# Optimization experiments

Hardware: AMD Instinct MI355X
Metric: run time of the kernel (lower is better)

The kernel has to match this reference:

```python
import jax, jax.numpy as jnp
import numpy as np

B, S, L, C, H, W_IMG = 4, 2, 1024, 128, 256, 256
HEADS1, D1 = 4, C // 4          # layer 1: 4 heads x 32 dims, concat
HEADS2, D2 = 1, C               # layer 2: 1 head x 128 dims, mean
LN_EPS = 1e-5
NEG_SLOPE = 0.2


def _xavier(k, shape):
    limit = float(np.sqrt(6.0 / (shape[0] + shape[1])))
    return jax.random.uniform(k, shape, jnp.float32, -limit, limit)


def setup_inputs() -> dict:
    key = jax.random.key(0)
    ks = jax.random.split(key, 10)
    seg_feats = jax.random.normal(ks[0], (B, S, L, C), jnp.float32)
    # integer segment labels in 0..L (0 = background), stored per forward spec
    seg_images = jax.random.randint(ks[1], (B, S, H, W_IMG), 0, L + 1, jnp.int32)
    seg_nums = jnp.full((B, S), L, jnp.int32)
    return {
        "seg_feats": seg_feats,
        "seg_images": seg_images,
        "seg_nums": seg_nums,
        "W1": _xavier(ks[2], (HEADS1 * D1, C)),   # Linear weight (out, in)
        "a_src1": _xavier(ks[3], (HEADS1, D1)),
        "a_dst1": _xavier(ks[4], (HEADS1, D1)),
        "W2": _xavier(ks[5], (HEADS2 * D2, C)),
        "a_src2": _xavier(ks[6], (HEADS2, D2)),
        "a_dst2": _xavier(ks[7], (HEADS2, D2)),
        "ln_gamma": jnp.ones((C,), jnp.float32),
        "ln_beta": jnp.zeros((C,), jnp.float32),
    }


def build_adjacency(seg):
    """seg: (H, W) int labels in 1..L (0 = background) -> (L, L) float adj with self-loops."""
    adj = jnp.eye(L, dtype=jnp.float32)

    def add_edges(adj, a, b):
        valid = (a > 0) & (b > 0) & (a != b)
        ai = jnp.clip(a - 1, 0, L - 1)
        bi = jnp.clip(b - 1, 0, L - 1)
        v = valid.astype(jnp.float32)
        adj = adj.at[ai, bi].max(v)
        return adj.at[bi, ai].max(v)

    pairs = [
        (seg[:, :-1], seg[:, 1:]),       # horizontal
        (seg[:-1, :], seg[1:, :]),       # vertical
        (seg[:-1, :-1], seg[1:, 1:]),    # diagonal \
        (seg[:-1, 1:], seg[1:, :-1]),    # diagonal /
    ]
    for a, b in pairs:
        adj = add_edges(adj, a.reshape(-1), b.reshape(-1))
    return adj


def _leaky_relu(x):
    return jnp.where(x >= 0, x, NEG_SLOPE * x)


def gat_layer(x, adj, W, a_src, a_dst, heads, d, concat):
    N = x.shape[0]
    Wf = (x @ W.T).reshape(N, heads, d)                     # (N, h, d)
    e_src = jnp.einsum('nhd,hd->nh', Wf, a_src)             # (N, h)
    e_dst = jnp.einsum('nhd,hd->nh', Wf, a_dst)             # (N, h)
    e = _leaky_relu(e_src[:, None, :] + e_dst[None, :, :])  # (N, N, h)
    e = jnp.where((adj == 0)[:, :, None], -jnp.inf, e)
    alpha = jax.nn.softmax(e, axis=1)                       # softmax over neighbours j
    h = jnp.einsum('ijh,jhd->ihd', alpha, Wf)               # (N, h, d)
    if concat:
        return jax.nn.elu(h.reshape(N, heads * d))
    return h.mean(axis=1)


def reference(seg_feats, seg_images, seg_nums, W1, a_src1, a_dst1,
              W2, a_src2, a_dst2, ln_gamma, ln_beta):
    feats = seg_feats.reshape(B * S, L, C)
    adjs = jax.vmap(build_adjacency)(seg_images.reshape(B * S, H, W_IMG))

    def enrich(f, adj):
        h = gat_layer(f, adj, W1, a_src1, a_dst1, HEADS1, D1, True)
        h = gat_layer(h, adj, W2, a_src2, a_dst2, HEADS2, D2, False)
        y = f + h
        mu = jnp.mean(y, axis=-1, keepdims=True)
        var = jnp.var(y, axis=-1, keepdims=True)
        return (y - mu) * jax.lax.rsqrt(var + LN_EPS) * ln_gamma + ln_beta

    out = jax.vmap(enrich)(feats, adjs)
    return out.reshape(B, S, L, C)
```

## Files before the change

### kernel.cpp

```cpp
#include <hip/hip_runtime.h>
#include <hip/hip_bf16.h>
#include <stdint.h>

#define LL 1024
#define CC 128
#define NG 8
#define NN (NG*LL)
typedef __hip_bfloat16 bf16;
typedef __attribute__((ext_vector_type(8))) short short8;
typedef __attribute__((ext_vector_type(4))) short short4v;
typedef __attribute__((ext_vector_type(4))) float f32x4;

__device__ __forceinline__ bool is_bf16_wire(const void* gamma) {
  return *(const uint32_t*)gamma == 0x3F803F80u;
}
__device__ __forceinline__ float ldw(const void* p, size_t i, bool bf) {
  return bf ? __bfloat162float(((const bf16*)p)[i]) : ((const float*)p)[i];
}
__device__ __forceinline__ uint32_t encf(float f) {
  uint32_t b = __float_as_uint(f);
  return (b & 0x80000000u) ? ~b : (b | 0x80000000u);
}
__device__ __forceinline__ float decf(uint32_t u) {
  return (u & 0x80000000u) ? __uint_as_float(u & 0x7FFFFFFFu) : __uint_as_float(~u);
}
__device__ __forceinline__ short f2bs(float x) {
  uint32_t u = __float_as_uint(x);
  u += 0x7FFFu + ((u >> 16) & 1u);
  return (short)(u >> 16);
}
template <bool BFW>
__device__ __forceinline__ short8 ld8w(const void* p, size_t off) {
  if (BFW) {
    return *(const short8*)((const bf16*)p + off);
  } else {
    const float4* f = (const float4*)((const float*)p + off);
    float4 a = f[0], b = f[1];
    short8 r;
    r[0] = f2bs(a.x); r[1] = f2bs(a.y); r[2] = f2bs(a.z); r[3] = f2bs(a.w);
    r[4] = f2bs(b.x); r[5] = f2bs(b.y); r[6] = f2bs(b.z); r[7] = f2bs(b.w);
    return r;
  }
}


template <int NH, bool BFW>
__device__ __forceinline__ void gemm_split(const short8 af[4],
    const void* __restrict__ Wsrc, const void* __restrict__ as_,
    const void* __restrict__ ad_, bf16* __restrict__ WfT,
    float* __restrict__ es, float* __restrict__ ed,
    uint32_t* __restrict__ edmax, int n0, int lane, int w,
    float* __restrict__ lds_red) {
  int quad = lane >> 4, c = lane & 15;
  int g = n0 >> 10;
  int dt0 = w * 2;
  f32x4 acc[2];
  acc[0] = (f32x4){0.f, 0.f, 0.f, 0.f};
  acc[1] = (f32x4){0.f, 0.f, 0.f, 0.f};
#pragma unroll
  for (int ks = 0; ks < 4; ks++)
#pragma unroll
    for (int d2 = 0; d2 < 2; d2++) {
      short8 bfr = ld8w<BFW>(Wsrc, (size_t)((dt0 + d2) * 16 + c) * CC + ks * 32 + quad * 8);
      acc[d2] = __builtin_amdgcn_mfma_f32_16x16x32_bf16(af[ks], bfr, acc[d2], 0, 0, 0);
    }
  {
    int nw4 = ((n0 & 1023) >> 2) + quad;
    bf16* wdst = WfT + (size_t)g * 131072 + (size_t)nw4 * 512 + c * 4;
#pragma unroll
    for (int d2 = 0; d2 < 2; d2++) {
      short4v pk;
#pragma unroll
      for (int r = 0; r < 4; r++) pk[r] = f2bs(acc[d2][r]);
      *(short4v*)&wdst[(dt0 + d2) * 64] = pk;
    }
  }
  float sv[4] = {0.f, 0.f, 0.f, 0.f}, dv[4] = {0.f, 0.f, 0.f, 0.f};
#pragma unroll
  for (int d2 = 0; d2 < 2; d2++) {
    int o = (dt0 + d2) * 16 + c;
    float a_s = ldw(as_, o, BFW);
    float a_d = ldw(ad_, o, BFW);
#pragma unroll
    for (int r = 0; r < 4; r++) {
      sv[r] += acc[d2][r] * a_s;
      dv[r] += acc[d2][r] * a_d;
    }
  }
#pragma unroll
  for (int m = 1; m <= 8; m <<= 1)
#pragma unroll
    for (int r = 0; r < 4; r++) {
      sv[r] += __shfl_xor(sv[r], m);
      dv[r] += __shfl_xor(dv[r], m);
    }
  if (NH == 4) {
    if (c == 0)
#pragma unroll
      for (int r = 0; r < 4; r++) {
        int node = n0 + quad * 4 + r;
        es[node * 4 + w] = sv[r];
        ed[node * 4 + w] = dv[r];
      }
    float mq = fmaxf(fmaxf(dv[0], dv[1]), fmaxf(dv[2], dv[3]));
    mq = fmaxf(mq, __shfl_xor(mq, 16));
    mq = fmaxf(mq, __shfl_xor(mq, 32));
    if (lane == 0) atomicMax(&edmax[g * 4 + w], encf(mq));
  } else {
    if (c == 0)
#pragma unroll
      for (int r = 0; r < 4; r++) {
        int nl = quad * 4 + r;
        lds_red[(w * 16 + nl) * 2 + 0] = sv[r];
        lds_red[(w * 16 + nl) * 2 + 1] = dv[r];
      }
    __syncthreads();
    if (w == 0) {
      int nl = lane & 15;
      float se = 0.f, de = 0.f;
#pragma unroll
      for (int ww = 0; ww < 4; ww++) {
        se += lds_red[(ww * 16 + nl) * 2 + 0];
        de += lds_red[(ww * 16 + nl) * 2 + 1];
      }
      if (lane < 16) { es[n0 + nl] = se; ed[n0 + nl] = de; }
      float mq = de;
      mq = fmaxf(mq, __shfl_xor(mq, 1));
      mq = fmaxf(mq, __shfl_xor(mq, 2));
      mq = fmaxf(mq, __shfl_xor(mq, 4));
      mq = fmaxf(mq, __shfl_xor(mq, 8));
      if (lane == 0) atomicMax(&edmax[g], encf(mq));
    }
  }
}

template <bool BFW>
__device__ __forceinline__ void gemm1_body(const void* __restrict__ feats,
    const void* __restrict__ W1, const void* __restrict__ as1,
    const void* __restrict__ ad1, bf16* __restrict__ WfT,
    float* __restrict__ es, float* __restrict__ ed,
    uint32_t* __restrict__ edmax, int bb, int t) {
  int lane = t & 63, w = t >> 6;
  int quad = lane >> 4, c = lane & 15;
  int n0 = (bb & 7) * 1024 + (bb >> 3) * 16;
  short8 af[4];
#pragma unroll
  for (int ks = 0; ks < 4; ks++)
    af[ks] = ld8w<BFW>(feats, (size_t)(n0 + c) * CC + ks * 32 + quad * 8);
  gemm_split<4, BFW>(af, W1, as1, ad1, WfT, es, ed, edmax, n0, lane, w, nullptr);
}

__global__ __launch_bounds__(256) void k_front(
    const void* __restrict__ feats, const void* __restrict__ W1,
    const void* __restrict__ as1, const void* __restrict__ ad1,
    const void* __restrict__ gamma, const int* __restrict__ img,
    uint8_t* __restrict__ adj, bf16* __restrict__ WfT,
    float* __restrict__ es, float* __restrict__ ed,
    uint32_t* __restrict__ edmax) {
  int bid = blockIdx.x;
  if (bid < 512) {
    if (is_bf16_wire(gamma))
      gemm1_body<true>(feats, W1, as1, ad1, WfT, es, ed, edmax, bid, threadIdx.x);
    else
      gemm1_body<false>(feats, W1, as1, ad1, WfT, es, ed, edmax, bid, threadIdx.x);
    return;
  }
  int rel = bid - 512;
  int g = rel & 7;
  int y = rel >> 3;
  int x = threadIdx.x;
  int p = y * 256 + x;
  const int* im = img + g * 65536;
  uint8_t* A = adj + ((size_t)g << 20);
  int a = im[p];
  if (a > 0) {
    int nxs[4] = {x + 1, x, x + 1, x - 1};
    int nys[4] = {y, y + 1, y + 1, y + 1};
#pragma unroll
    for (int d = 0; d < 4; d++) {
      int nx = nxs[d], ny = nys[d];
      if (nx < 0 || nx > 255 || ny > 255) continue;
      int b = im[ny * 256 + nx];
      if (b > 0 && b != a) {
        A[(size_t)(a - 1) * LL + (b - 1)] = 1;
      }
    }
  }
}

template <int NH>
__global__ __launch_bounds__(256) void k_attn(
    const bf16* __restrict__ WfT, const float* __restrict__ esb,
    const float* __restrict__ edb, const uint8_t* __restrict__ adjb,
    const uint32_t* __restrict__ edmax, bf16* __restrict__ pacc,
    float* __restrict__ pml) {
  __shared__ __align__(16) float smem[8320];
  __shared__ float lred[4][16 * NH];
  uint8_t* scol = (uint8_t*)smem;
  float* eds = smem + 2560;
  float* red = smem;
  int t = threadIdx.x;
  int lane = t & 63, w = t >> 6;
  int quad = lane >> 4, c = lane & 15;
  int bid = blockIdx.x;
  int g = bid & 7, jp = (bid >> 3) & 1, rt = bid >> 4;
  int i0 = rt * 16;
  int node = g * LL + i0 + c;
  int J0 = jp * 512 + w * 128;
  for (int u = t; u < 512 * NH; u += 256) {
    int h = u >> 9, j = u & 511;
    eds[h * 520 + j] = edb[(size_t)(g * LL + jp * 512 + j) * NH + h];
  }
  for (int u = t; u < 512; u += 256) {
    const uint8_t* src = adjb + ((size_t)g << 20) + (size_t)(jp * 512 + u) * 1024 + i0;
    uint4 v = *(const uint4*)src;
    uint32_t* dst = (uint32_t*)&scol[u * 20];
    dst[0] = v.x; dst[1] = v.y; dst[2] = v.z; dst[3] = v.w;
  }
  const float LOG2E = 1.44269504f;
  float esv[NH], cmv[NH];
  if (NH == 4) {
    const float4 e4 = *(const float4*)&esb[(size_t)node * 4];
    esv[0] = e4.x; esv[1] = e4.y; esv[2] = e4.z; esv[3] = e4.w;
  } else {
    esv[0] = esb[node];
  }
#pragma unroll
  for (int h = 0; h < NH; h++) {
    float mx = decf(edmax[NH == 4 ? g * 4 + h : g]);
    float m = esv[h] + mx; m = fmaxf(m, 0.2f * m);
    cmv[h] = -m * LOG2E;
  }
  int rowg = i0 + c;
  const uint8_t* arow = adjb + ((size_t)g << 20) + (size_t)rowg * 1024 + jp * 512 + w * 128;
  uint2 mbj[4];
#pragma unroll
  for (int jb = 0; jb < 4; jb++)
    mbj[jb] = *(const uint2*)&arow[jb * 32 + quad * 8];
  f32x4 acc[8];
#pragma unroll
  for (int dt = 0; dt < 8; dt++) acc[dt] = (f32x4){0.f, 0.f, 0.f, 0.f};
  float lsum[NH];
#pragma unroll
  for (int h = 0; h < NH; h++) lsum[h] = 0.f;
  const bf16* wb = WfT + (size_t)g * 131072 + (size_t)J0 * 128 + quad * 1024 + c * 4;
  __syncthreads();

  union FB { uint2 u[2]; short8 s; };
#pragma unroll
  for (int jb = 0; jb < 4; jb++) {
    short8 frag[8];
#pragma unroll
    for (int dt = 0; dt < 8; dt++) {
      FB f;
      f.u[0] = *(const uint2*)&wb[jb * 4096 + dt * 64];
      f.u[1] = *(const uint2*)&wb[jb * 4096 + dt * 64 + 512];
      frag[dt] = f.s;
    }
    int base_wj = w * 128 + jb * 32 + quad * 8;
    int jg0 = jp * 512 + base_wj;
    uint32_t bx = mbj[jb].x, by = mbj[jb].y;
    float mf[8];
#pragma unroll
    for (int i = 0; i < 8; i++) {
      uint32_t bit = (i < 4) ? ((bx >> (8 * i)) & 1u) : ((by >> (8 * (i - 4))) & 1u);
      uint32_t cb = scol[(base_wj + i) * 20 + c];
      uint32_t mm = bit | cb | (uint32_t)(jg0 + i == rowg);
      mf[i] = (float)(mm != 0u);
    }
#pragma unroll
    for (int h = 0; h < NH; h++) {
      const float* ep = &eds[h * 520 + base_wj];
      float4 ea = *(const float4*)ep;
      float4 eb = *(const float4*)(ep + 4);
      float ev[8] = {ea.x, ea.y, ea.z, ea.w, eb.x, eb.y, eb.z, eb.w};
      float pr[8];
      float lac = 0.f;
#pragma unroll
      for (int i = 0; i < 8; i++) {
        float e = esv[h] + ev[i];
        e = fmaxf(e, 0.2f * e);
        float p = exp2f(fmaf(e, LOG2E, cmv[h]));
        p *= mf[i];
        lac += p;
        pr[i] = p;
      }
      lsum[h] += lac;
      union { short8 s; uint32_t u[4]; } A;
#pragma unroll
      for (int k = 0; k < 4; k++) {
        __hip_bfloat162 q = __float22bfloat162_rn(make_float2(pr[2*k], pr[2*k+1]));
        A.u[k] = *reinterpret_cast<uint32_t*>(&q);
      }
#pragma unroll
      for (int d2 = 0; d2 < 8 / NH; d2++) {
        int dt = h * (8 / NH) + d2;
        acc[dt] = __builtin_amdgcn_mfma_f32_16x16x32_bf16(A.s, frag[dt], acc[dt], 0, 0, 0);
      }
    }
  }
#pragma unroll
  for (int h = 0; h < NH; h++) {
    float v = lsum[h];
    v += __shfl_xor(v, 16);
    v += __shfl_xor(v, 32);
    lsum[h] = v;
  }
  if (quad == 0)
#pragma unroll
    for (int h = 0; h < NH; h++) lred[w][c * NH + h] = lsum[h];
  __syncthreads();
  if (w >= 1)
#pragma unroll
    for (int dt = 0; dt < 8; dt++)
      *(f32x4*)&red[(w - 1) * 2048 + dt * 256 + lane * 4] = acc[dt];
  __syncthreads();
  if (w == 0) {
#pragma unroll
    for (int dt = 0; dt < 8; dt++) {
      acc[dt] += *(const f32x4*)&red[dt * 256 + lane * 4];
      acc[dt] += *(const f32x4*)&red[2048 + dt * 256 + lane * 4];
      acc[dt] += *(const f32x4*)&red[4096 + dt * 256 + lane * 4];
    }
#pragma unroll
    for (int dt = 0; dt < 8; dt++)
#pragma unroll
      for (int r = 0; r < 4; r++)
        red[6144 + (quad * 4 + r) * 132 + dt * 16 + c] = acc[dt][r];
  }
  __syncthreads();
  {
    int row = t >> 4, d0 = (t & 15) * 8;
    const float* src = &red[6144 + row * 132 + d0];
    short8 pk;
#pragma unroll
    for (int k = 0; k < 8; k++) pk[k] = f2bs(src[k]);
    *(short8*)&pacc[((size_t)jp * NN + g * LL + i0 + row) * CC + d0] = pk;
  }
  if (t < 16 * NH) {
    float l = lred[0][t] + lred[1][t] + lred[2][t] + lred[3][t];
    int row = (NH == 4) ? (t >> 2) : t;
    int h = (NH == 4) ? (t & 3) : 0;
    if (NH == 4) pml[((size_t)jp * NN + g * LL + i0 + row) * 4 + h] = l;
    else         pml[(size_t)jp * NN + g * LL + i0 + row] = l;
  }
}

template <bool BFW>
__device__ __forceinline__ void gemm2_body(const bf16* __restrict__ pacc,
    const float* __restrict__ pml1, const void* __restrict__ W2,
    const void* __restrict__ as2, const void* __restrict__ ad2,
    bf16* __restrict__ WfT, float* __restrict__ es, float* __restrict__ ed,
    uint32_t* __restrict__ edmax, float* __restrict__ lds_red,
    int bid, int t) {
  int lane = t & 63, w = t >> 6;
  int quad = lane >> 4, c = lane & 15;
  int n0 = (bid & 7) * 1024 + (bid >> 3) * 16;
  int node = n0 + c;
  float4 l4 = make_float4(0.f, 0.f, 0.f, 0.f);
#pragma unroll
  for (int p = 0; p < 2; p++) {
    float4 v = *(const float4*)&pml1[((size_t)p * NN + node) * 4];
    l4.x += v.x; l4.y += v.y; l4.z += v.z; l4.w += v.w;
  }
  float linv[4] = {1.f / l4.x, 1.f / l4.y, 1.f / l4.z, 1.f / l4.w};
  short8 af[4];
#pragma unroll
  for (int ks = 0; ks < 4; ks++) {
    float a[8] = {0.f, 0.f, 0.f, 0.f, 0.f, 0.f, 0.f, 0.f};
#pragma unroll
    for (int p = 0; p < 2; p++) {
      short8 v = *(const short8*)&pacc[((size_t)p * NN + node) * CC + ks * 32 + quad * 8];
#pragma unroll
      for (int i = 0; i < 8; i++) {
        union { short s[2]; float f; } cv; cv.s[0] = 0; cv.s[1] = v[i];
        a[i] += cv.f;
      }
    }
#pragma unroll
    for (int i = 0; i < 8; i++) {
      float vv = a[i] * linv[ks];
      vv = (vv > 0.f) ? vv : (__expf(vv) - 1.f);
      af[ks][i] = f2bs(vv);
    }
  }
  gemm_split<1, BFW>(af, W2, as2, ad2, WfT, es, ed, edmax, n0, lane, w, lds_red);
}

__global__ __launch_bounds__(256) void k_gemm2c(
    const bf16* __restrict__ pacc, const float* __restrict__ pml1,
    const void* __restrict__ W2, const void* __restrict__ as2,
    const void* __restrict__ ad2, const void* __restrict__ gamma,
    bf16* __restrict__ WfT, float* __restrict__ es, float* __restrict__ ed,
    uint32_t* __restrict__ edmax) {
  __shared__ float lds_red[128];
  if (is_bf16_wire(gamma))
    gemm2_body<true>(pacc, pml1, W2, as2, ad2, WfT, es, ed, edmax, lds_red,
                     blockIdx.x, threadIdx.x);
  else
    gemm2_body<false>(pacc, pml1, W2, as2, ad2, WfT, es, ed, edmax, lds_red,
                      blockIdx.x, threadIdx.x);
}

__global__ __launch_bounds__(256) void k_combine2(const bf16* __restrict__ pacc,
    const float* __restrict__ pml2, const void* __restrict__ feats,
    const void* __restrict__ gamma, const void* __restrict__ beta,
    void* __restrict__ outp) {
  const bool bf = is_bf16_wire(gamma);
  int t = threadIdx.x;
  int node = (blockIdx.x & 7) * 1024 + (blockIdx.x >> 3) * 4 + (t >> 6);
  int lane = t & 63;
  float l = 0.f, a0 = 0.f, a1 = 0.f;
#pragma unroll
  for (int p = 0; p < 2; p++) {
    l  += pml2[(size_t)p * NN + node];
    a0 += __bfloat162float(pacc[((size_t)p * NN + node) * CC + lane]);
    a1 += __bfloat162float(pacc[((size_t)p * NN + node) * CC + 64 + lane]);
  }
  float y0 = ldw(feats, (size_t)node * CC + lane, bf) + a0 / l;
  float y1 = ldw(feats, (size_t)node * CC + 64 + lane, bf) + a1 / l;
  float s = y0 + y1, s2 = y0 * y0 + y1 * y1;
#pragma unroll
  for (int mm = 32; mm >= 1; mm >>= 1) { s += __shfl_xor(s, mm); s2 += __shfl_xor(s2, mm); }
  float mu = s * (1.f / 128.f);
  float var = fmaxf(s2 * (1.f / 128.f) - mu * mu, 0.f);
  float rs = rsqrtf(var + 1e-5f);
  float o0 = (y0 - mu) * rs * ldw(gamma, lane, bf) + ldw(beta, lane, bf);
  float o1 = (y1 - mu) * rs * ldw(gamma, 64 + lane, bf) + ldw(beta, 64 + lane, bf);
  if (bf) {
    ((bf16*)outp)[(size_t)node * CC + lane]      = __float2bfloat16(o0);
    ((bf16*)outp)[(size_t)node * CC + 64 + lane] = __float2bfloat16(o1);
  } else {
    ((float*)outp)[(size_t)node * CC + lane]      = o0;
    ((float*)outp)[(size_t)node * CC + 64 + lane] = o1;
  }
}

extern "C" void kernel_launch(void* const* d_in, const int* in_sizes, int n_in,
                              void* d_out, int out_size, void* d_ws, size_t ws_size,
                              hipStream_t stream) {
  const void* feats = d_in[0];
  const int*  imgs  = (const int*)d_in[1];
  const void* W1    = d_in[3];
  const void* as1   = d_in[4];
  const void* ad1   = d_in[5];
  const void* W2    = d_in[6];
  const void* as2   = d_in[7];
  const void* ad2   = d_in[8];
  const void* gamma = d_in[9];
  const void* beta  = d_in[10];

  char* ws = (char*)d_ws;
  uint8_t*  adj    = (uint8_t*)ws;
  uint32_t* edmax1 = (uint32_t*)(ws + 8388608);
  uint32_t* edmax2 = (uint32_t*)(ws + 8388736);
  bf16*     WfT    = (bf16*)(ws + 8519680);
  float*    es1    = (float*)(ws + 10616832);
  float*    ed1    = (float*)(ws + 10747904);
  float*    es2    = (float*)(ws + 10878976);
  float*    ed2    = (float*)(ws + 10911744);
  float*    pml    = (float*)(ws + 10944512);
  bf16*     pacc   = (bf16*)(ws + 11206656);

  hipMemsetAsync(ws, 0, 8389120, stream);
  hipLaunchKernelGGL(k_front, dim3(2560), dim3(256), 0, stream,
                     feats, W1, as1, ad1, gamma, imgs,
                     adj, WfT, es1, ed1, edmax1);
  hipLaunchKernelGGL((k_attn<4>), dim3(1024), dim3(256), 0, stream,
                     WfT, es1, ed1, adj, edmax1, pacc, pml);
  hipLaunchKernelGGL(k_gemm2c, dim3(512), dim3(256), 0, stream,
                     pacc, pml, W2, as2, ad2, gamma, WfT, es2, ed2, edmax2);
  hipLaunchKernelGGL((k_attn<1>), dim3(1024), dim3(256), 0, stream,
                     WfT, es2, ed2, adj, edmax2, pacc, pml);
  hipLaunchKernelGGL(k_combine2, dim3(2048), dim3(256), 0, stream,
                     pacc, pml, feats, gamma, beta, d_out);
}
```

Before: 168.1 us.

## Symmetrize adjacency at build time and process two row tiles per attention block

The adjacency builder now writes both (a,b) and (b,a) entries, so the attention kernel no longer stages a transposed column slice of the mask in shared memory and ORs it in. Each attention block now covers 32 query rows (two 16-row MFMA tiles) instead of 16. The WfT fragments and destination scores loaded per block are shared across both tiles, and the grid is halved. The trade-off is twice the scattered byte writes in the adjacency build and more accumulator registers per thread (two sets of 8 f32x4), which may reduce occupancy. The epilogue reduction now runs once per tile with extra barriers.

```diff
diff --git a/kernel.cpp b/kernel.cpp
--- a/kernel.cpp
+++ b/kernel.cpp
@@ -183,6 +183,7 @@
       int b = im[ny * 256 + nx];
       if (b > 0 && b != a) {
         A[(size_t)(a - 1) * LL + (b - 1)] = 1;
+        A[(size_t)(b - 1) * LL + (a - 1)] = 1;
       }
     }
   }
@@ -195,54 +196,54 @@
     const uint32_t* __restrict__ edmax, bf16* __restrict__ pacc,
     float* __restrict__ pml) {
   __shared__ __align__(16) float smem[8320];
-  __shared__ float lred[4][16 * NH];
-  uint8_t* scol = (uint8_t*)smem;
-  float* eds = smem + 2560;
+  __shared__ float lred[2][4][16 * NH];
+  float* eds = smem;
   float* red = smem;
   int t = threadIdx.x;
   int lane = t & 63, w = t >> 6;
   int quad = lane >> 4, c = lane & 15;
   int bid = blockIdx.x;
   int g = bid & 7, jp = (bid >> 3) & 1, rt = bid >> 4;
-  int i0 = rt * 16;
-  int node = g * LL + i0 + c;
+  int i0 = rt * 32;
   int J0 = jp * 512 + w * 128;
   for (int u = t; u < 512 * NH; u += 256) {
     int h = u >> 9, j = u & 511;
     eds[h * 520 + j] = edb[(size_t)(g * LL + jp * 512 + j) * NH + h];
   }
-  for (int u = t; u < 512; u += 256) {
-    const uint8_t* src = adjb + ((size_t)g << 20) + (size_t)(jp * 512 + u) * 1024 + i0;
-    uint4 v = *(const uint4*)src;
-    uint32_t* dst = (uint32_t*)&scol[u * 20];
-    dst[0] = v.x; dst[1] = v.y; dst[2] = v.z; dst[3] = v.w;
-  }
   const float LOG2E = 1.44269504f;
-  float esv[NH], cmv[NH];
-  if (NH == 4) {
-    const float4 e4 = *(const float4*)&esb[(size_t)node * 4];
-    esv[0] = e4.x; esv[1] = e4.y; esv[2] = e4.z; esv[3] = e4.w;
-  } else {
-    esv[0] = esb[node];
-  }
-#pragma unroll
-  for (int h = 0; h < NH; h++) {
-    float mx = decf(edmax[NH == 4 ? g * 4 + h : g]);
-    float m = esv[h] + mx; m = fmaxf(m, 0.2f * m);
-    cmv[h] = -m * LOG2E;
-  }
-  int rowg = i0 + c;
-  const uint8_t* arow = adjb + ((size_t)g << 20) + (size_t)rowg * 1024 + jp * 512 + w * 128;
-  uint2 mbj[4];
-#pragma unroll
-  for (int jb = 0; jb < 4; jb++)
-    mbj[jb] = *(const uint2*)&arow[jb * 32 + quad * 8];
-  f32x4 acc[8];
-#pragma unroll
-  for (int dt = 0; dt < 8; dt++) acc[dt] = (f32x4){0.f, 0.f, 0.f, 0.f};
-  float lsum[NH];
-#pragma unroll
-  for (int h = 0; h < NH; h++) lsum[h] = 0.f;
+  float esv[2][NH], cmv[2][NH];
+  {
+    float mxh[NH];
+#pragma unroll
+    for (int h = 0; h < NH; h++) mxh[h] = decf(edmax[NH == 4 ? g * 4 + h : g]);
+#pragma unroll
+    for (int tr = 0; tr < 2; tr++) {
+      int node = g * LL + i0 + tr * 16 + c;
+      if (NH == 4) {
+        float4 e4 = *(const float4*)&esb[(size_t)node * 4];
+        esv[tr][0] = e4.x; esv[tr][1] = e4.y; esv[tr][2] = e4.z; esv[tr][3] = e4.w;
+      } else {
+        esv[tr][0] = esb[node];
+      }
+#pragma unroll
+      for (int h = 0; h < NH; h++) {
+        float m = esv[tr][h] + mxh[h]; m = fmaxf(m, 0.2f * m);
+        cmv[tr][h] = -m * LOG2E;
+      }
+    }
+  }
+  int row0 = i0 + c;
+  const uint8_t* arow0 = adjb + ((size_t)g << 20) + (size_t)row0 * 1024 + jp * 512 + w * 128;
+  f32x4 acc[2][8];
+#pragma unroll
+  for (int tr = 0; tr < 2; tr++)
+#pragma unroll
+    for (int dt = 0; dt < 8; dt++) acc[tr][dt] = (f32x4){0.f, 0.f, 0.f, 0.f};
+  float lsum[2][NH];
+#pragma unroll
+  for (int tr = 0; tr < 2; tr++)
+#pragma unroll
+    for (int h = 0; h < NH; h++) lsum[tr][h] = 0.f;
   const bf16* wb = WfT + (size_t)g * 131072 + (size_t)J0 * 128 + quad * 1024 + c * 4;
   __syncthreads();
 
@@ -257,16 +258,21 @@
       f.u[1] = *(const uint2*)&wb[jb * 4096 + dt * 64 + 512];
       frag[dt] = f.s;
     }
+    uint2 mb[2];
+    mb[0] = *(const uint2*)&arow0[jb * 32 + quad * 8];
+    mb[1] = *(const uint2*)&arow0[16384 + jb * 32 + quad * 8];
     int base_wj = w * 128 + jb * 32 + quad * 8;
     int jg0 = jp * 512 + base_wj;
-    uint32_t bx = mbj[jb].x, by = mbj[jb].y;
-    float mf[8];
-#pragma unroll
-    for (int i = 0; i < 8; i++) {
-      uint32_t bit = (i < 4) ? ((bx >> (8 * i)) & 1u) : ((by >> (8 * (i - 4))) & 1u);
-      uint32_t cb = scol[(base_wj + i) * 20 + c];
-      uint32_t mm = bit | cb | (uint32_t)(jg0 + i == rowg);
-      mf[i] = (float)(mm != 0u);
+    float mf[2][8];
+#pragma unroll
+    for (int tr = 0; tr < 2; tr++) {
+      uint32_t bx = mb[tr].x, by = mb[tr].y;
+      int rg = row0 + tr * 16;
+#pragma unroll
+      for (int i = 0; i < 8; i++) {
+        uint32_t bit = (i < 4) ? ((bx >> (8 * i)) & 1u) : ((by >> (8 * (i - 4))) & 1u);
+        mf[tr][i] = (float)(bit | (uint32_t)(jg0 + i == rg));
+      }
     }
 #pragma unroll
     for (int h = 0; h < NH; h++) {
@@ -274,75 +280,80 @@
       float4 ea = *(const float4*)ep;
       float4 eb = *(const float4*)(ep + 4);
       float ev[8] = {ea.x, ea.y, ea.z, ea.w, eb.x, eb.y, eb.z, eb.w};
-      float pr[8];
-      float lac = 0.f;
-#pragma unroll
-      for (int i = 0; i < 8; i++) {
-        float e = esv[h] + ev[i];
-        e = fmaxf(e, 0.2f * e);
-        float p = exp2f(fmaf(e, LOG2E, cmv[h]));
-        p *= mf[i];
-        lac += p;
-        pr[i] = p;
-      }
-      lsum[h] += lac;
-      union { short8 s; uint32_t u[4]; } A;
-#pragma unroll
-      for (int k = 0; k < 4; k++) {
-        __hip_bfloat162 q = __float22bfloat162_rn(make_float2(pr[2*k], pr[2*k+1]));
-        A.u[k] = *reinterpret_cast<uint32_t*>(&q);
-      }
-#pragma unroll
-      for (int d2 = 0; d2 < 8 / NH; d2++) {
-        int dt = h * (8 / NH) + d2;
-        acc[dt] = __builtin_amdgcn_mfma_f32_16x16x32_bf16(A.s, frag[dt], acc[dt], 0, 0, 0);
-      }
-    }
-  }
-#pragma unroll
-  for (int h = 0; h < NH; h++) {
-    float v = lsum[h];
-    v += __shfl_xor(v, 16);
-    v += __shfl_xor(v, 32);
-    lsum[h] = v;
-  }
-  if (quad == 0)
-#pragma unroll
-    for (int h = 0; h < NH; h++) lred[w][c * NH + h] = lsum[h];
+#pragma unroll
+      for (int tr = 0; tr < 2; tr++) {
+        float pr[8];
+        float lac = 0.f;
+#pragma unroll
+        for (int i = 0; i < 8; i++) {
+          float e = esv[tr][h] + ev[i];
+          e = fmaxf(e, 0.2f * e);
+          float p = exp2f(fmaf(e, LOG2E, cmv[tr][h]));
+          p *= mf[tr][i];
+          lac += p;
+          pr[i] = p;
+        }
+        lsum[tr][h] += lac;
+        union { short8 s; uint32_t u[4]; } A;
+#pragma unroll
+        for (int k = 0; k < 4; k++) {
+          __hip_bfloat162 q = __float22bfloat162_rn(make_float2(pr[2*k], pr[2*k+1]));
+          A.u[k] = *reinterpret_cast<uint32_t*>(&q);
+        }
+#pragma unroll
+        for (int d2 = 0; d2 < 8 / NH; d2++) {
+          int dt = h * (8 / NH) + d2;
+          acc[tr][dt] = __builtin_amdgcn_mfma_f32_16x16x32_bf16(A.s, frag[dt], acc[tr][dt], 0, 0, 0);
+        }
+      }
+    }
+  }
+#pragma unroll
+  for (int tr = 0; tr < 2; tr++)
+#pragma unroll
+    for (int h = 0; h < NH; h++) {
+      float v = lsum[tr][h];
+      v += __shfl_xor(v, 16);
+      v += __shfl_xor(v, 32);
+      if (quad == 0) lred[tr][w][c * NH + h] = v;
+    }
   __syncthreads();
-  if (w >= 1)
-#pragma unroll
-    for (int dt = 0; dt < 8; dt++)
-      *(f32x4*)&red[(w - 1) * 2048 + dt * 256 + lane * 4] = acc[dt];
-  __syncthreads();
-  if (w == 0) {
-#pragma unroll
-    for (int dt = 0; dt < 8; dt++) {
-      acc[dt] += *(const f32x4*)&red[dt * 256 + lane * 4];
-      acc[dt] += *(const f32x4*)&red[2048 + dt * 256 + lane * 4];
-      acc[dt] += *(const f32x4*)&red[4096 + dt * 256 + lane * 4];
-    }
-#pragma unroll
-    for (int dt = 0; dt < 8; dt++)
-#pragma unroll
-      for (int r = 0; r < 4; r++)
-        red[6144 + (quad * 4 + r) * 132 + dt * 16 + c] = acc[dt][r];
-  }
-  __syncthreads();
-  {
-    int row = t >> 4, d0 = (t & 15) * 8;
-    const float* src = &red[6144 + row * 132 + d0];
-    short8 pk;
-#pragma unroll
-    for (int k = 0; k < 8; k++) pk[k] = f2bs(src[k]);
-    *(short8*)&pacc[((size_t)jp * NN + g * LL + i0 + row) * CC + d0] = pk;
-  }
-  if (t < 16 * NH) {
-    float l = lred[0][t] + lred[1][t] + lred[2][t] + lred[3][t];
-    int row = (NH == 4) ? (t >> 2) : t;
-    int h = (NH == 4) ? (t & 3) : 0;
-    if (NH == 4) pml[((size_t)jp * NN + g * LL + i0 + row) * 4 + h] = l;
-    else         pml[(size_t)jp * NN + g * LL + i0 + row] = l;
+#pragma unroll
+  for (int tr = 0; tr < 2; tr++) {
+    if (w >= 1)
+#pragma unroll
+      for (int dt = 0; dt < 8; dt++)
+        *(f32x4*)&red[(w - 1) * 2048 + dt * 256 + lane * 4] = acc[tr][dt];
+    __syncthreads();
+    if (w == 0) {
+#pragma unroll
+      for (int dt = 0; dt < 8; dt++) {
+        f32x4 s = acc[tr][dt];
+        s += *(const f32x4*)&red[dt * 256 + lane * 4];
+        s += *(const f32x4*)&red[2048 + dt * 256 + lane * 4];
+        s += *(const f32x4*)&red[4096 + dt * 256 + lane * 4];
+#pragma unroll
+        for (int r = 0; r < 4; r++)
+          red[6144 + (quad * 4 + r) * 132 + dt * 16 + c] = s[r];
+      }
+    }
+    __syncthreads();
+    {
+      int row = t >> 4, d0 = (t & 15) * 8;
+      const float* src = &red[6144 + row * 132 + d0];
+      short8 pk;
+#pragma unroll
+      for (int k = 0; k < 8; k++) pk[k] = f2bs(src[k]);
+      *(short8*)&pacc[((size_t)jp * NN + g * LL + i0 + tr * 16 + row) * CC + d0] = pk;
+    }
+    if (t < 16 * NH) {
+      float l = lred[tr][0][t] + lred[tr][1][t] + lred[tr][2][t] + lred[tr][3][t];
+      int row = (NH == 4) ? (t >> 2) : t;
+      int h = (NH == 4) ? (t & 3) : 0;
+      if (NH == 4) pml[((size_t)jp * NN + g * LL + i0 + tr * 16 + row) * 4 + h] = l;
+      else         pml[(size_t)jp * NN + g * LL + i0 + tr * 16 + row] = l;
+    }
+    __syncthreads();
   }
 }
 
@@ -466,11 +477,11 @@
   hipLaunchKernelGGL(k_front, dim3(2560), dim3(256), 0, stream,
                      feats, W1, as1, ad1, gamma, imgs,
                      adj, WfT, es1, ed1, edmax1);
-  hipLaunchKernelGGL((k_attn<4>), dim3(1024), dim3(256), 0, stream,
+  hipLaunchKernelGGL((k_attn<4>), dim3(512), dim3(256), 0, stream,
                      WfT, es1, ed1, adj, edmax1, pacc, pml);
   hipLaunchKernelGGL(k_gemm2c, dim3(512), dim3(256), 0, stream,
                      pacc, pml, W2, as2, ad2, gamma, WfT, es2, ed2, edmax2);
-  hipLaunchKernelGGL((k_attn<1>), dim3(1024), dim3(256), 0, stream,
+  hipLaunchKernelGGL((k_attn<1>), dim3(512), dim3(256), 0, stream,
                      WfT, es2, ed2, adj, edmax2, pacc, pml);
   hipLaunchKernelGGL(k_combine2, dim3(2048), dim3(256), 0, stream,
                      pacc, pml, feats, gamma, beta, d_out);
```

After: 176.4 us. 1.05x slower.
